# Performance work log

Hardware: AMD Instinct MI355X
Metric: run time of the kernel (lower is better)

## Reference

```python
import jax, jax.numpy as jnp
import numpy as np

MB, NUM, LENTH, SIZE, OUT = 16, 128, 64, 256, 256
DIN = (LENTH + 1) * 2  # aux_lenth = 0


def setup_inputs() -> dict:
    key = jax.random.key(0)
    ks = jax.random.split(key, 9)
    s = 0.05
    return {
        "in_": jax.random.normal(ks[0], (MB, NUM, LENTH), dtype=jnp.float32),
        "W1": jax.random.normal(ks[1], (DIN, SIZE), dtype=jnp.float32) * s,
        "b1": jax.random.normal(ks[2], (SIZE,), dtype=jnp.float32) * s,
        "W2": jax.random.normal(ks[3], (SIZE, SIZE), dtype=jnp.float32) * s,
        "b2": jax.random.normal(ks[4], (SIZE,), dtype=jnp.float32) * s,
        "W3": jax.random.normal(ks[5], (SIZE, SIZE), dtype=jnp.float32) * s,
        "b3": jax.random.normal(ks[6], (SIZE,), dtype=jnp.float32) * s,
        "W4": jax.random.normal(ks[7], (SIZE, OUT), dtype=jnp.float32) * s,
        "b4": jax.random.normal(ks[8], (OUT,), dtype=jnp.float32) * s,
    }


def reference(in_, W1, b1, W2, b2, W3, b3, W4, b4):
    mb, num, _ = in_.shape
    # append coordinate channel: coord[i] = i  -> [mb, num, lenth+1]
    coord = jnp.broadcast_to(
        jnp.arange(num, dtype=in_.dtype)[None, :, None], (mb, num, 1)
    )
    x = jnp.concatenate([in_, coord], axis=2)  # [mb, num, L1], L1 = lenth+1
    L1 = x.shape[2]
    # pairwise: x_full[b, a, j] = concat(x[b, j], x[b, a])
    x_i = jnp.broadcast_to(x[:, None, :, :], (mb, num, num, L1))  # varies over j
    x_j = jnp.broadcast_to(x[:, :, None, :], (mb, num, num, L1))  # varies over a
    x_full = jnp.concatenate([x_i, x_j], axis=3)  # [mb, num, num, 2*L1]
    h = x_full.reshape(mb * num * num, 2 * L1)
    h = jax.nn.relu(h @ W1 + b1)
    h = jax.nn.relu(h @ W2 + b2)
    h = jax.nn.relu(h @ W3 + b3)
    h = jax.nn.relu(h @ W4 + b4)  # [mb*num*num, OUT]
    x_g = h.reshape(mb, num * num, -1).sum(axis=1)  # [mb, OUT]
    return x_g
```

## Files before the change

kernel.cpp:

```cpp
#include <hip/hip_runtime.h>
#include <hip/hip_bf16.h>

using short8 = __attribute__((ext_vector_type(8))) short;
using f32x4  = __attribute__((ext_vector_type(4))) float;

#define MBATCH 16
#define NUMV   128
#define LEN    64
#define SZ     256

__device__ __forceinline__ unsigned short bfbits(float x) {
  union { float f; unsigned u; } c; c.f = x;
  return (unsigned short)((c.u + 0x8000u) >> 16);
}

__global__ void uv_prep(const float* __restrict__ in_, const float* __restrict__ W1,
                        const float* __restrict__ b1,
                        float* __restrict__ u, float* __restrict__ v) {
  int bn = blockIdx.x;
  int n  = bn & (NUMV - 1);
  int s  = threadIdx.x;
  __shared__ float xs[LEN];
  if (s < LEN) xs[s] = in_[bn * LEN + s];
  __syncthreads();
  float fn = (float)n;
  float uu = fn * W1[64 * SZ + s];
  float vv = fn * W1[129 * SZ + s] + b1[s];
  for (int c = 0; c < LEN; ++c) {
    uu = fmaf(xs[c], W1[c * SZ + s], uu);
    vv = fmaf(xs[c], W1[(65 + c) * SZ + s], vv);
  }
  u[bn * SZ + s] = uu;
  v[bn * SZ + s] = vv;
}

__global__ void w_prep(const float* __restrict__ W2, const float* __restrict__ W3,
                       const float* __restrict__ W4, short* __restrict__ wlay) {
  int L = blockIdx.x >> 3, kb = blockIdx.x & 7;
  const float* W = (L == 0) ? W2 : (L == 1) ? W3 : W4;
  int m = threadIdx.x >> 6, lane = threadIdx.x & 63;
  int l16 = lane & 15, q = lane >> 4;
  for (int wv = 0; wv < 4; ++wv) {
    int ch = wv * 64 + m * 16 + l16;
    short8 pk;
    for (int i = 0; i < 8; ++i)
      pk[i] = (short)bfbits(W[(kb * 32 + q * 8 + i) * SZ + ch]);
    int f = ((L * 8 + kb) * 4 + wv) * 4 + m;
    reinterpret_cast<short8*>(wlay)[f * 64 + lane] = pk;
  }
}

__global__ __launch_bounds__(256, 3) void fused_mlp(
    const float* __restrict__ u, const float* __restrict__ v,
    const short* __restrict__ wlay,
    const float* __restrict__ b2, const float* __restrict__ b3, const float* __restrict__ b4,
    float* __restrict__ partial) {
  __shared__ __align__(16) short hbuf[64 * 256];

  int wg = blockIdx.x;
  int b = wg >> 8, a = (wg >> 1) & 127, jh = wg & 1;
  int tid = threadIdx.x;
  int wave = tid >> 6, lane = tid & 63;
  int l16 = lane & 15, q = lane >> 4;

  const char* wptr = (const char*)wlay + wave * 4096 + lane * 16;

  short8 awA[4], awB[4];
  #pragma unroll
  for (int m = 0; m < 4; ++m)
    awA[m] = *reinterpret_cast<const short8*>(wptr + m * 1024);

  {
    const float4* ub = (const float4*)(u + (size_t)b * NUMV * SZ) + jh * 64 * 64;
    const float4* vb = (const float4*)(v + ((size_t)b * NUMV + a) * SZ);
    #pragma unroll
    for (int it = 0; it < 16; ++it) {
      int flat = tid + it * 256;
      int jr = flat >> 6, c4 = flat & 63;
      float4 uu = ub[jr * 64 + c4];
      float4 vv = vb[c4];
      unsigned lo = (unsigned)bfbits(fmaxf(uu.x + vv.x, 0.f))
                  | ((unsigned)bfbits(fmaxf(uu.y + vv.y, 0.f)) << 16);
      unsigned hi = (unsigned)bfbits(fmaxf(uu.z + vv.z, 0.f))
                  | ((unsigned)bfbits(fmaxf(uu.w + vv.w, 0.f)) << 16);
      int byte = (jr * 512 + c4 * 8) ^ ((jr & 7) << 4);
      uint2 pk; pk.x = lo; pk.y = hi;
      *reinterpret_cast<uint2*>((char*)hbuf + byte) = pk;
    }
  }

  __syncthreads();

  #pragma unroll
  for (int L = 0; L < 3; ++L) {
    const float* bb = (L == 0) ? b2 : (L == 1) ? b3 : b4;

    f32x4 acc[4][4];
    #pragma unroll
    for (int m = 0; m < 4; ++m)
      #pragma unroll
      for (int n = 0; n < 4; ++n)
        acc[m][n] = f32x4{0.f, 0.f, 0.f, 0.f};

    #pragma unroll
    for (int kb = 0; kb < 8; ++kb) {
      if (L * 8 + kb < 23) {
        if ((kb & 1) == 0) {
          #pragma unroll
          for (int m = 0; m < 4; ++m)
            awB[m] = *reinterpret_cast<const short8*>(wptr + 16384 + m * 1024);
        } else {
          #pragma unroll
          for (int m = 0; m < 4; ++m)
            awA[m] = *reinterpret_cast<const short8*>(wptr + 16384 + m * 1024);
        }
      }
      wptr += 16384;

      short8 bfr0, bfr1, bfr2, bfr3;
      {
        int row0 = 0 * 16 + l16, row1 = 1 * 16 + l16;
        bfr0 = *reinterpret_cast<const short8*>((char*)hbuf +
               ((row0 * 512 + kb * 64 + q * 16) ^ ((row0 & 7) << 4)));
        bfr1 = *reinterpret_cast<const short8*>((char*)hbuf +
               ((row1 * 512 + kb * 64 + q * 16) ^ ((row1 & 7) << 4)));
      }
      if ((kb & 1) == 0) {
        #pragma unroll
        for (int m = 0; m < 4; ++m) {
          acc[m][0] = __builtin_amdgcn_mfma_f32_16x16x32_bf16(awA[m], bfr0, acc[m][0], 0, 0, 0);
          acc[m][1] = __builtin_amdgcn_mfma_f32_16x16x32_bf16(awA[m], bfr1, acc[m][1], 0, 0, 0);
        }
      } else {
        #pragma unroll
        for (int m = 0; m < 4; ++m) {
          acc[m][0] = __builtin_amdgcn_mfma_f32_16x16x32_bf16(awB[m], bfr0, acc[m][0], 0, 0, 0);
          acc[m][1] = __builtin_amdgcn_mfma_f32_16x16x32_bf16(awB[m], bfr1, acc[m][1], 0, 0, 0);
        }
      }
      {
        int row2 = 2 * 16 + l16, row3 = 3 * 16 + l16;
        bfr2 = *reinterpret_cast<const short8*>((char*)hbuf +
               ((row2 * 512 + kb * 64 + q * 16) ^ ((row2 & 7) << 4)));
        bfr3 = *reinterpret_cast<const short8*>((char*)hbuf +
               ((row3 * 512 + kb * 64 + q * 16) ^ ((row3 & 7) << 4)));
      }
      if ((kb & 1) == 0) {
        #pragma unroll
        for (int m = 0; m < 4; ++m) {
          acc[m][2] = __builtin_amdgcn_mfma_f32_16x16x32_bf16(awA[m], bfr2, acc[m][2], 0, 0, 0);
          acc[m][3] = __builtin_amdgcn_mfma_f32_16x16x32_bf16(awA[m], bfr3, acc[m][3], 0, 0, 0);
        }
      } else {
        #pragma unroll
        for (int m = 0; m < 4; ++m) {
          acc[m][2] = __builtin_amdgcn_mfma_f32_16x16x32_bf16(awB[m], bfr2, acc[m][2], 0, 0, 0);
          acc[m][3] = __builtin_amdgcn_mfma_f32_16x16x32_bf16(awB[m], bfr3, acc[m][3], 0, 0, 0);
        }
      }
    }

    __syncthreads();

    if (L < 2) {
      #pragma unroll
      for (int m = 0; m < 4; ++m) {
        f32x4 bv = *reinterpret_cast<const f32x4*>(bb + wave * 64 + m * 16 + q * 4);
        int ch = wave * 64 + m * 16 + q * 4;
        #pragma unroll
        for (int n = 0; n < 4; ++n) {
          int row = n * 16 + l16;
          f32x4 t = acc[m][n];
          unsigned lo = (unsigned)bfbits(fmaxf(t[0] + bv[0], 0.f))
                      | ((unsigned)bfbits(fmaxf(t[1] + bv[1], 0.f)) << 16);
          unsigned hi = (unsigned)bfbits(fmaxf(t[2] + bv[2], 0.f))
                      | ((unsigned)bfbits(fmaxf(t[3] + bv[3], 0.f)) << 16);
          int byte = (row * 512 + ch * 2) ^ ((row & 7) << 4);
          uint2 pk; pk.x = lo; pk.y = hi;
          *reinterpret_cast<uint2*>((char*)hbuf + byte) = pk;
        }
      }
      __syncthreads();
    } else {
      #pragma unroll
      for (int m = 0; m < 4; ++m) {
        f32x4 bv = *reinterpret_cast<const f32x4*>(bb + wave * 64 + m * 16 + q * 4);
        f32x4 s = f32x4{0.f, 0.f, 0.f, 0.f};
        #pragma unroll
        for (int n = 0; n < 4; ++n) {
          s[0] += fmaxf(acc[m][n][0] + bv[0], 0.f);
          s[1] += fmaxf(acc[m][n][1] + bv[1], 0.f);
          s[2] += fmaxf(acc[m][n][2] + bv[2], 0.f);
          s[3] += fmaxf(acc[m][n][3] + bv[3], 0.f);
        }
        #pragma unroll
        for (int r = 0; r < 4; ++r) {
          float x = s[r];
          x += __shfl_xor(x, 1);
          x += __shfl_xor(x, 2);
          x += __shfl_xor(x, 4);
          x += __shfl_xor(x, 8);
          s[r] = x;
        }
        if (l16 == 0) {
          float4 o; o.x = s[0]; o.y = s[1]; o.z = s[2]; o.w = s[3];
          *reinterpret_cast<float4*>(partial + (size_t)wg * SZ + wave * 64 + m * 16 + q * 4) = o;
        }
      }
    }
  }
}

__global__ void reduce_partials(const float* __restrict__ partial, float* __restrict__ out) {
  int b = blockIdx.x;
  int s = threadIdx.x;
  const float* p = partial + (size_t)b * 256 * SZ + s;
  float acc = 0.f;
  for (int i = 0; i < 256; ++i) acc += p[(size_t)i * SZ];
  out[b * SZ + s] = acc;
}

extern "C" void kernel_launch(void* const* d_in, const int* in_sizes, int n_in,
                              void* d_out, int out_size, void* d_ws, size_t ws_size,
                              hipStream_t stream) {
  const float* in_ = (const float*)d_in[0];
  const float* W1  = (const float*)d_in[1];
  const float* b1  = (const float*)d_in[2];
  const float* W2  = (const float*)d_in[3];
  const float* b2  = (const float*)d_in[4];
  const float* W3  = (const float*)d_in[5];
  const float* b3  = (const float*)d_in[6];
  const float* W4  = (const float*)d_in[7];
  const float* b4  = (const float*)d_in[8];
  float* out = (float*)d_out;

  char* ws = (char*)d_ws;
  float* u       = (float*)(ws);
  float* v       = (float*)(ws + (2u << 20));
  short* wlay    = (short*)(ws + (4u << 20));
  float* partial = (float*)(ws + (4u << 20) + (1u << 19));

  uv_prep<<<MBATCH * NUMV, 256, 0, stream>>>(in_, W1, b1, u, v);
  w_prep<<<24, 256, 0, stream>>>(W2, W3, W4, wlay);
  fused_mlp<<<MBATCH * NUMV * 2, 256, 0, stream>>>(u, v, wlay, b2, b3, b4, partial);
  reduce_partials<<<MBATCH, 256, 0, stream>>>(partial, out);
}
```

Baseline: 126.1 us.

## Merge row halves into one 512-thread block per (batch, a) pair

Each workgroup now covers all 128 j rows with 8 waves, split as 4 channel groups by 2 row halves, in place of two 256-thread blocks that each covered 64 rows. Both row halves share the per-block weight fragment stream from L2. The two halves' partial sums are combined in LDS before a single global write, which halves the partial buffer and the final reduction work. The cost is 64KB of LDS per block with occupancy bounded at 2 blocks, and fewer blocks in the grid.

Result: slower. 135.7 us (+7.6%).

```diff
diff --git a/kernel.cpp b/kernel.cpp
--- a/kernel.cpp
+++ b/kernel.cpp
@@ -50,20 +50,21 @@
   }
 }
 
-__global__ __launch_bounds__(256, 3) void fused_mlp(
+__global__ __launch_bounds__(512, 2) void fused_mlp(
     const float* __restrict__ u, const float* __restrict__ v,
     const short* __restrict__ wlay,
     const float* __restrict__ b2, const float* __restrict__ b3, const float* __restrict__ b4,
     float* __restrict__ partial) {
-  __shared__ __align__(16) short hbuf[64 * 256];
+  __shared__ __align__(16) short hbuf[128 * 256];
 
   int wg = blockIdx.x;
-  int b = wg >> 8, a = (wg >> 1) & 127, jh = wg & 1;
+  int b = wg >> 7, a = wg & 127;
   int tid = threadIdx.x;
   int wave = tid >> 6, lane = tid & 63;
+  int wch = wave & 3, wrow = wave >> 2;
   int l16 = lane & 15, q = lane >> 4;
 
-  const char* wptr = (const char*)wlay + wave * 4096 + lane * 16;
+  const char* wptr = (const char*)wlay + wch * 4096 + lane * 16;
 
   short8 awA[4], awB[4];
   #pragma unroll
@@ -71,11 +72,11 @@
     awA[m] = *reinterpret_cast<const short8*>(wptr + m * 1024);
 
   {
-    const float4* ub = (const float4*)(u + (size_t)b * NUMV * SZ) + jh * 64 * 64;
+    const float4* ub = (const float4*)(u + (size_t)b * NUMV * SZ);
     const float4* vb = (const float4*)(v + ((size_t)b * NUMV + a) * SZ);
     #pragma unroll
     for (int it = 0; it < 16; ++it) {
-      int flat = tid + it * 256;
+      int flat = tid + it * 512;
       int jr = flat >> 6, c4 = flat & 63;
       float4 uu = ub[jr * 64 + c4];
       float4 vv = vb[c4];
@@ -119,7 +120,7 @@
 
       short8 bfr0, bfr1, bfr2, bfr3;
       {
-        int row0 = 0 * 16 + l16, row1 = 1 * 16 + l16;
+        int row0 = wrow * 64 + 0 * 16 + l16, row1 = wrow * 64 + 1 * 16 + l16;
         bfr0 = *reinterpret_cast<const short8*>((char*)hbuf +
                ((row0 * 512 + kb * 64 + q * 16) ^ ((row0 & 7) << 4)));
         bfr1 = *reinterpret_cast<const short8*>((char*)hbuf +
@@ -139,7 +140,7 @@
         }
       }
       {
-        int row2 = 2 * 16 + l16, row3 = 3 * 16 + l16;
+        int row2 = wrow * 64 + 2 * 16 + l16, row3 = wrow * 64 + 3 * 16 + l16;
         bfr2 = *reinterpret_cast<const short8*>((char*)hbuf +
                ((row2 * 512 + kb * 64 + q * 16) ^ ((row2 & 7) << 4)));
         bfr3 = *reinterpret_cast<const short8*>((char*)hbuf +
@@ -165,11 +166,11 @@
     if (L < 2) {
       #pragma unroll
       for (int m = 0; m < 4; ++m) {
-        f32x4 bv = *reinterpret_cast<const f32x4*>(bb + wave * 64 + m * 16 + q * 4);
-        int ch = wave * 64 + m * 16 + q * 4;
+        f32x4 bv = *reinterpret_cast<const f32x4*>(bb + wch * 64 + m * 16 + q * 4);
+        int ch = wch * 64 + m * 16 + q * 4;
         #pragma unroll
         for (int n = 0; n < 4; ++n) {
-          int row = n * 16 + l16;
+          int row = wrow * 64 + n * 16 + l16;
           f32x4 t = acc[m][n];
           unsigned lo = (unsigned)bfbits(fmaxf(t[0] + bv[0], 0.f))
                       | ((unsigned)bfbits(fmaxf(t[1] + bv[1], 0.f)) << 16);
@@ -182,9 +183,10 @@
       }
       __syncthreads();
     } else {
+      float* pbuf = (float*)hbuf;
       #pragma unroll
       for (int m = 0; m < 4; ++m) {
-        f32x4 bv = *reinterpret_cast<const f32x4*>(bb + wave * 64 + m * 16 + q * 4);
+        f32x4 bv = *reinterpret_cast<const f32x4*>(bb + wch * 64 + m * 16 + q * 4);
         f32x4 s = f32x4{0.f, 0.f, 0.f, 0.f};
         #pragma unroll
         for (int n = 0; n < 4; ++n) {
@@ -204,9 +206,12 @@
         }
         if (l16 == 0) {
           float4 o; o.x = s[0]; o.y = s[1]; o.z = s[2]; o.w = s[3];
-          *reinterpret_cast<float4*>(partial + (size_t)wg * SZ + wave * 64 + m * 16 + q * 4) = o;
-        }
-      }
+          *reinterpret_cast<float4*>(pbuf + wrow * 256 + wch * 64 + m * 16 + q * 4) = o;
+        }
+      }
+      __syncthreads();
+      if (tid < 256)
+        partial[(size_t)wg * SZ + tid] = pbuf[tid] + pbuf[256 + tid];
     }
   }
 }
@@ -214,9 +219,9 @@
 __global__ void reduce_partials(const float* __restrict__ partial, float* __restrict__ out) {
   int b = blockIdx.x;
   int s = threadIdx.x;
-  const float* p = partial + (size_t)b * 256 * SZ + s;
+  const float* p = partial + (size_t)b * NUMV * SZ + s;
   float acc = 0.f;
-  for (int i = 0; i < 256; ++i) acc += p[(size_t)i * SZ];
+  for (int i = 0; i < NUMV; ++i) acc += p[(size_t)i * SZ];
   out[b * SZ + s] = acc;
 }
 
@@ -242,6 +247,6 @@
 
   uv_prep<<<MBATCH * NUMV, 256, 0, stream>>>(in_, W1, b1, u, v);
   w_prep<<<24, 256, 0, stream>>>(W2, W3, W4, wlay);
-  fused_mlp<<<MBATCH * NUMV * 2, 256, 0, stream>>>(u, v, wlay, b2, b3, b4, partial);
+  fused_mlp<<<MBATCH * NUMV, 512, 0, stream>>>(u, v, wlay, b2, b3, b4, partial);
   reduce_partials<<<MBATCH, 256, 0, stream>>>(partial, out);
 }
```
